# Performance work log

Hardware: AMD Instinct MI355X
Metric: run time of the kernel (lower is better)

## Reference

```python
import jax, jax.numpy as jnp
import numpy as np

D_MODEL = 1024
NUM_HEADS = 16
D_K = D_MODEL // NUM_HEADS


def setup_inputs() -> dict:
    key = jax.random.key(0)
    ks = jax.random.split(key, 7)
    B, S = 4, 2048
    lim = float(np.sqrt(6.0 / (D_MODEL + D_MODEL)))  # xavier uniform
    x = jax.random.normal(ks[0], (B, S, D_MODEL), dtype=jnp.float32)
    w_q = jax.random.uniform(ks[1], (D_MODEL, D_MODEL), jnp.float32, -lim, lim)
    w_k = jax.random.uniform(ks[2], (D_MODEL, D_MODEL), jnp.float32, -lim, lim)
    w_v = jax.random.uniform(ks[3], (D_MODEL, D_MODEL), jnp.float32, -lim, lim)
    w_o = jax.random.uniform(ks[4], (D_MODEL, D_MODEL), jnp.float32, -lim, lim)
    b_o = jnp.zeros((D_MODEL,), jnp.float32)
    ln_g = jnp.ones((D_MODEL,), jnp.float32)
    ln_b = jnp.zeros((D_MODEL,), jnp.float32)
    return {"x": x, "w_q": w_q, "w_k": w_k, "w_v": w_v, "w_o": w_o,
            "b_o": b_o, "ln_g": ln_g, "ln_b": ln_b}


def _layer_norm(y, g, b, eps=1e-5):
    mu = jnp.mean(y, axis=-1, keepdims=True)
    var = jnp.var(y, axis=-1, keepdims=True)
    return (y - mu) * jax.lax.rsqrt(var + eps) * g + b


def reference(x, w_q, w_k, w_v, w_o, b_o, ln_g, ln_b):
    B, S, D = x.shape
    # Linear weights stored torch-style [out, in]: y = x @ W^T
    def proj(w):
        return jnp.einsum('bsd,ed->bse', x, w).reshape(B, S, NUM_HEADS, D_K).transpose(0, 2, 1, 3)
    Q, K, V = proj(w_q), proj(w_k), proj(w_v)  # [B, H, S, d_k]
    scores = jnp.einsum('bhqd,bhkd->bhqk', Q, K) / jnp.sqrt(jnp.float32(D_K))
    attn = jax.nn.softmax(scores, axis=-1)  # dropout identity at eval
    out = jnp.einsum('bhqk,bhkd->bhqd', attn, V)  # [B, H, S, d_k]
    out = out.transpose(0, 2, 1, 3).reshape(B, S, D)
    out = jnp.einsum('bsd,ed->bse', out, w_o) + b_o
    return _layer_norm(x + out, ln_g, ln_b)
```

## Files before the change

kernel.cpp:

```cpp
#include <hip/hip_runtime.h>

typedef __bf16 bf16;
typedef bf16 v8bf __attribute__((ext_vector_type(8)));
typedef bf16 v4bf __attribute__((ext_vector_type(4)));
typedef float v4f __attribute__((ext_vector_type(4)));
typedef float v16f __attribute__((ext_vector_type(16)));
typedef unsigned int u32;
typedef u32 v4u __attribute__((ext_vector_type(4)));

#define GAS __attribute__((address_space(1)))
#define LAS __attribute__((address_space(3)))

constexpr int D    = 1024;
constexpr int ROWS = 8192;
constexpr int TILE = 128;

__global__ __launch_bounds__(256) void cast_all(
    const float* __restrict__ x,
    const float* __restrict__ wq, const float* __restrict__ wk,
    const float* __restrict__ wv, const float* __restrict__ wo,
    bf16* __restrict__ xb, bf16* __restrict__ wqb, bf16* __restrict__ wkb,
    bf16* __restrict__ wvb, bf16* __restrict__ wob)
{
    int i = blockIdx.x * 256 + threadIdx.x;
    const float* src; bf16* dst; int off;
    if (i < 2 * 1024 * 1024) { src = x; dst = xb; off = i; }
    else {
        int j = i - 2 * 1024 * 1024;
        int w = j >> 18;
        off = j & ((1 << 18) - 1);
        src = (w == 0) ? wq : (w == 1) ? wk : (w == 2) ? wv : wo;
        dst = (w == 0) ? wqb : (w == 1) ? wkb : (w == 2) ? wvb : wob;
    }
    float4 v = ((const float4*)src)[off];
    v4bf o;
    o[0] = (bf16)v.x; o[1] = (bf16)v.y; o[2] = (bf16)v.z; o[3] = (bf16)v.w;
    ((v4bf*)dst)[off] = o;
}

template<int MODE>
__global__ __launch_bounds__(256) void gemm_bt(
    const bf16* __restrict__ A,
    const bf16* __restrict__ W0, const bf16* __restrict__ W1, const bf16* __restrict__ W2,
    bf16* __restrict__ O0, bf16* __restrict__ O1, bf16* __restrict__ O2,
    float* __restrict__ Of, const float* __restrict__ bias,
    const float* __restrict__ X)
{
    __shared__ bf16 As[2][TILE * 32];
    __shared__ bf16 Bs[2][TILE * 32];

    const int tid  = threadIdx.x;
    const int lane = tid & 63;
    const int wave = tid >> 6;
    const int quad = lane >> 4;
    const int l16  = lane & 15;
    const int wm   = (wave >> 1) * 64;
    const int wn   = (wave & 1) * 64;

    const int z = blockIdx.z;
    const bf16* Bw = (MODE == 0) ? ((z == 0) ? W0 : ((z == 1) ? W1 : W2)) : W0;
    bf16*       Ob = (MODE == 0) ? ((z == 0) ? O0 : ((z == 1) ? O1 : O2)) : O0;

    const long rowA0 = (long)blockIdx.y * TILE;
    const long rowB0 = (long)blockIdx.x * TILE;

    const int stRow = wave * 16 + (lane >> 2);
    const int stCol = (lane & 3) * 8;
    const bf16* gA = A  + (rowA0 + stRow) * D + stCol;
    const bf16* gB = Bw + (rowB0 + stRow) * D + stCol;
    const int ldsOff = wave * 16 * 32;

    const v4f vzero = {0.f, 0.f, 0.f, 0.f};
    v4f acc[4][4];
    #pragma unroll
    for (int i = 0; i < 4; i++)
        #pragma unroll
        for (int j = 0; j < 4; j++) acc[i][j] = vzero;

    for (int k0 = 0; k0 < D; k0 += 64) {
        __syncthreads();
        #pragma unroll
        for (int p = 0; p < 2; ++p)
            #pragma unroll
            for (int i = 0; i < 2; ++i) {
                __builtin_amdgcn_global_load_lds(
                    (const GAS void*)(gA + (long)i * 64 * D + p * 32),
                    (LAS void*)(&As[p][ldsOff + i * 64 * 32]), 16, 0, 0);
                __builtin_amdgcn_global_load_lds(
                    (const GAS void*)(gB + (long)i * 64 * D + p * 32),
                    (LAS void*)(&Bs[p][ldsOff + i * 64 * 32]), 16, 0, 0);
            }
        gA += 64; gB += 64;
        __syncthreads();

        #pragma unroll
        for (int p = 0; p < 2; ++p) {
            v8bf a[4], b[4];
            #pragma unroll
            for (int mi = 0; mi < 4; mi++)
                a[mi] = *(const v8bf*)(&As[p][(wm + mi * 16 + l16) * 32 + quad * 8]);
            #pragma unroll
            for (int ni = 0; ni < 4; ni++)
                b[ni] = *(const v8bf*)(&Bs[p][(wn + ni * 16 + l16) * 32 + quad * 8]);
            #pragma unroll
            for (int mi = 0; mi < 4; mi++)
                #pragma unroll
                for (int ni = 0; ni < 4; ni++)
                    acc[mi][ni] = __builtin_amdgcn_mfma_f32_16x16x32_bf16(a[mi], b[ni], acc[mi][ni], 0, 0, 0);
        }
    }

    const float qscale = 0.125f * 1.44269504f;

    if (MODE == 0 && z == 2) {
        #pragma unroll
        for (int mi = 0; mi < 4; mi++) {
            #pragma unroll
            for (int ni = 0; ni < 4; ni++) {
                const long col = rowB0 + wn + ni * 16 + l16;
                const long h_ = col >> 6, dd = col & 63;
                const long row0 = rowA0 + wm + mi * 16 + quad * 4;
                const long b_ = row0 >> 11, s0 = row0 & 2047;
                v4bf pk;
                #pragma unroll
                for (int r = 0; r < 4; r++) pk[r] = (bf16)acc[mi][ni][r];
                *(v4bf*)(Ob + ((b_ * 16 + h_) * 64 + dd) * 2048 + s0) = pk;
            }
        }
    } else {
        #pragma unroll
        for (int mi = 0; mi < 4; mi++) {
            #pragma unroll
            for (int ni = 0; ni < 4; ni++) {
                const long col = rowB0 + wn + ni * 16 + l16;
                float bv = (MODE == 1) ? bias[col] : 0.f;
                #pragma unroll
                for (int r = 0; r < 4; r++) {
                    const long row = rowA0 + wm + mi * 16 + quad * 4 + r;
                    float v = acc[mi][ni][r];
                    if (MODE == 1) Of[row * D + col] = v + bv + X[row * D + col];
                    else {
                        if (z == 0) v *= qscale;
                        Ob[row * D + col] = (bf16)v;
                    }
                }
            }
        }
    }
}

__global__ __launch_bounds__(256) void attn_kernel(
    const bf16* __restrict__ Q, const bf16* __restrict__ Kg,
    const bf16* __restrict__ VtG, bf16* __restrict__ O)
{
    const int id  = blockIdx.x;
    const int xcd = id & 7, j = id >> 3;
    const int qt  = j & 15;
    const int g   = xcd + 8 * (j >> 4);
    const int h   = g & 15, b = g >> 4;

    const int tid  = threadIdx.x;
    const int lane = tid & 63;
    const int wave = tid >> 6;
    const int l31  = lane & 31;
    const int hi   = lane >> 5;

    __shared__ bf16 Kt[2][64 * 64];
    __shared__ bf16 Vt[2][64 * 64];

    const long qrow = (long)(b * 2048 + qt * 128 + wave * 32 + l31);
    v8bf qB[4];
    #pragma unroll
    for (int f = 0; f < 4; f++)
        qB[f] = *(const v8bf*)(Q + qrow * D + h * 64 + f * 16 + hi * 8);

    const v16f z16 = {0.f,0.f,0.f,0.f,0.f,0.f,0.f,0.f,
                      0.f,0.f,0.f,0.f,0.f,0.f,0.f,0.f};
    v16f o_acc[2];
    o_acc[0] = z16; o_acc[1] = z16;
    float l0 = 0.f, l1 = 0.f;

    const int iR = tid >> 3;
    const int c8 = tid & 7;
    const int sC = c8 * 8;
    const bf16* kLane = Kg  + (long)b * 2048 * D + h * 64 + sC + (long)iR * D;
    const bf16* vLane = VtG + (long)(b * 16 + h) * 64 * 2048 + sC + (long)iR * 2048;
    const int wOff = iR * 64 + ((c8 ^ (iR & 7)) * 8);

    v8bf kpre[2], vpre[2];
    kpre[0] = *(const v8bf*)(kLane);
    kpre[1] = *(const v8bf*)(kLane + 32 * D);
    vpre[0] = *(const v8bf*)(vLane);
    vpre[1] = *(const v8bf*)(vLane + 32 * 2048);
    kLane += 64 * D; vLane += 64;
    *(v8bf*)(&Kt[0][wOff])           = kpre[0];
    *(v8bf*)(&Kt[0][wOff + 32 * 64]) = kpre[1];
    *(v8bf*)(&Vt[0][wOff])           = vpre[0];
    *(v8bf*)(&Vt[0][wOff + 32 * 64]) = vpre[1];
    kpre[0] = *(const v8bf*)(kLane);
    kpre[1] = *(const v8bf*)(kLane + 32 * D);
    vpre[0] = *(const v8bf*)(vLane);
    vpre[1] = *(const v8bf*)(vLane + 32 * 2048);
    kLane += 64 * D; vLane += 64;

    for (int kt = 0; kt < 32; ++kt) {
        const int cur = kt & 1;
        __syncthreads();

        if (kt + 1 < 32) {
            *(v8bf*)(&Kt[cur ^ 1][wOff])           = kpre[0];
            *(v8bf*)(&Kt[cur ^ 1][wOff + 32 * 64]) = kpre[1];
            *(v8bf*)(&Vt[cur ^ 1][wOff])           = vpre[0];
            *(v8bf*)(&Vt[cur ^ 1][wOff + 32 * 64]) = vpre[1];
        }
        if (kt + 2 < 32) {
            kpre[0] = *(const v8bf*)(kLane);
            kpre[1] = *(const v8bf*)(kLane + 32 * D);
            vpre[0] = *(const v8bf*)(vLane);
            vpre[1] = *(const v8bf*)(vLane + 32 * 2048);
            kLane += 64 * D; vLane += 64;
        }

        #pragma unroll
        for (int ko = 0; ko < 2; ko++) {
            const int krow = ko * 32 + l31;
            const int ksw  = krow & 7;
            v8bf kA0 = *(const v8bf*)(&Kt[cur][krow * 64 + (((0 + hi) ^ ksw) * 8)]);
            v16f st  = __builtin_amdgcn_mfma_f32_32x32x16_bf16(kA0, qB[0], z16, 0, 0, 0);
            #pragma unroll
            for (int f = 1; f < 4; f++) {
                v8bf kA = *(const v8bf*)(&Kt[cur][krow * 64 + (((2 * f + hi) ^ ksw) * 8)]);
                st = __builtin_amdgcn_mfma_f32_32x32x16_bf16(kA, qB[f], st, 0, 0, 0);
            }

            float p[16];
            #pragma unroll
            for (int r = 0; r < 16; r++) {
                p[r] = __builtin_amdgcn_exp2f(st[r]);
                if (r & 1) l1 += p[r]; else l0 += p[r];
            }

            #pragma unroll
            for (int u = 0; u < 2; u++) {
                const int s = ko * 2 + u;
                u32 a0, a1, b0, b1;
                asm("v_cvt_pk_bf16_f32 %0, %1, %2" : "=v"(a0) : "v"(p[u*8+0]), "v"(p[u*8+1]));
                asm("v_cvt_pk_bf16_f32 %0, %1, %2" : "=v"(a1) : "v"(p[u*8+2]), "v"(p[u*8+3]));
                asm("v_cvt_pk_bf16_f32 %0, %1, %2" : "=v"(b0) : "v"(p[u*8+4]), "v"(p[u*8+5]));
                asm("v_cvt_pk_bf16_f32 %0, %1, %2" : "=v"(b1) : "v"(p[u*8+6]), "v"(p[u*8+7]));
                asm("v_permlane32_swap_b32 %0, %1" : "+v"(a0), "+v"(b0));
                asm("v_permlane32_swap_b32 %0, %1" : "+v"(a1), "+v"(b1));
                v4u w; w[0] = a0; w[1] = a1; w[2] = b0; w[3] = b1;
                const v8bf pa = __builtin_bit_cast(v8bf, w);
                #pragma unroll
                for (int d2 = 0; d2 < 2; d2++) {
                    const int vrow = d2 * 32 + l31;
                    v8bf vb = *(const v8bf*)(&Vt[cur][vrow * 64 + (((2 * s + hi) ^ (vrow & 7)) * 8)]);
                    o_acc[d2] = __builtin_amdgcn_mfma_f32_32x32x16_bf16(pa, vb, o_acc[d2], 0, 0, 0);
                }
            }
        }
    }

    float l_acc = l0 + l1;
    l_acc += __shfl_xor(l_acc, 32);

    const long obase = (long)(b * 2048 + qt * 128 + wave * 32);
    #pragma unroll
    for (int r = 0; r < 16; r++) {
        const int qp = (r & 3) + 8 * (r >> 2) + 4 * hi;
        const float inv = 1.f / __shfl(l_acc, qp);
        O[(obase + qp) * D + h * 64 + l31]      = (bf16)(o_acc[0][r] * inv);
        O[(obase + qp) * D + h * 64 + 32 + l31] = (bf16)(o_acc[1][r] * inv);
    }
}

__global__ __launch_bounds__(256) void ln_kernel(
    const float* __restrict__ g, const float* __restrict__ beta,
    float* __restrict__ out)
{
    const int row = blockIdx.x;
    const int t = threadIdx.x;
    const int lane = t & 63, wave = t >> 6;
    const long base = (long)row * D + t * 4;

    float4 yv = *(const float4*)(out + base);
    float y0 = yv.x, y1 = yv.y, y2 = yv.z, y3 = yv.w;
    float s1 = y0 + y1 + y2 + y3;
    float s2 = y0*y0 + y1*y1 + y2*y2 + y3*y3;
    #pragma unroll
    for (int off = 1; off < 64; off <<= 1) {
        s1 += __shfl_xor(s1, off);
        s2 += __shfl_xor(s2, off);
    }
    __shared__ float r1[4], r2[4];
    if (lane == 0) { r1[wave] = s1; r2[wave] = s2; }
    __syncthreads();
    float S1 = r1[0] + r1[1] + r1[2] + r1[3];
    float S2 = r2[0] + r2[1] + r2[2] + r2[3];
    float mu  = S1 * (1.f / 1024.f);
    float var = S2 * (1.f / 1024.f) - mu * mu;
    float rsd = rsqrtf(var + 1e-5f);

    float4 gv = *(const float4*)(g + t * 4);
    float4 bv = *(const float4*)(beta + t * 4);
    float4 o;
    o.x = (y0 - mu) * rsd * gv.x + bv.x;
    o.y = (y1 - mu) * rsd * gv.y + bv.y;
    o.z = (y2 - mu) * rsd * gv.z + bv.z;
    o.w = (y3 - mu) * rsd * gv.w + bv.w;
    *(float4*)(out + base) = o;
}

extern "C" void kernel_launch(void* const* d_in, const int* in_sizes, int n_in,
                              void* d_out, int out_size, void* d_ws, size_t ws_size,
                              hipStream_t stream)
{
    const float* x   = (const float*)d_in[0];
    const float* wq  = (const float*)d_in[1];
    const float* wk  = (const float*)d_in[2];
    const float* wv  = (const float*)d_in[3];
    const float* wo  = (const float*)d_in[4];
    const float* bo  = (const float*)d_in[5];
    const float* lng = (const float*)d_in[6];
    const float* lnb = (const float*)d_in[7];
    float* out = (float*)d_out;

    char* ws = (char*)d_ws;
    bf16* xb  = (bf16*)(ws);
    bf16* wqb = (bf16*)(ws + (size_t)16 * 1024 * 1024);
    bf16* wkb = wqb + 1024 * 1024;
    bf16* wvb = wkb + 1024 * 1024;
    bf16* wob = wvb + 1024 * 1024;
    bf16* Qb  = (bf16*)(ws + (size_t)24 * 1024 * 1024);
    bf16* Kb  = Qb + (size_t)ROWS * D;
    bf16* VtG = Kb + (size_t)ROWS * D;
    bf16* Ab  = VtG + (size_t)ROWS * D;

    cast_all<<<12288, 256, 0, stream>>>(x, wq, wk, wv, wo,
                                        xb, wqb, wkb, wvb, wob);

    dim3 gqkv(D / TILE, ROWS / TILE, 3);
    gemm_bt<0><<<gqkv, 256, 0, stream>>>(xb, wqb, wkb, wvb, Qb, Kb, VtG,
                                         nullptr, nullptr, nullptr);

    attn_kernel<<<dim3(1024, 1, 1), 256, 0, stream>>>(Qb, Kb, VtG, Ab);

    dim3 gout(D / TILE, ROWS / TILE, 1);
    gemm_bt<1><<<gout, 256, 0, stream>>>(Ab, wob, nullptr, nullptr,
                                         nullptr, nullptr, nullptr, out, bo, x);

    ln_kernel<<<8192, 256, 0, stream>>>(lng, lnb, out);
}
```

Measured before the change: 299.9 us.

## Enlarge attention blocks to 512 threads, process two KV tiles per sync

The attention kernel now runs 512-thread blocks covering 256 query rows, so each K/V tile loaded into shared memory is reused by twice as many waves. The grid is halved to match. The loop is restructured so each barrier stages two 64-key tiles into a four-slot buffer, halving synchronisations per KV pass. K fragments are batched before the MFMA chain, and MFMA sections get raised wave priority via s_setprio. The cost is more LDS per block (32 KB) and higher register pressure under launch_bounds(512,4), which may reduce occupancy or cause spills.

```diff
diff --git a/kernel.cpp b/kernel.cpp
--- a/kernel.cpp
+++ b/kernel.cpp
@@ -149,14 +149,14 @@
     }
 }
 
-__global__ __launch_bounds__(256) void attn_kernel(
+__global__ __launch_bounds__(512, 4) void attn_kernel(
     const bf16* __restrict__ Q, const bf16* __restrict__ Kg,
     const bf16* __restrict__ VtG, bf16* __restrict__ O)
 {
     const int id  = blockIdx.x;
     const int xcd = id & 7, j = id >> 3;
-    const int qt  = j & 15;
-    const int g   = xcd + 8 * (j >> 4);
+    const int qt  = j & 7;
+    const int g   = xcd + 8 * (j >> 3);
     const int h   = g & 15, b = g >> 4;
 
     const int tid  = threadIdx.x;
@@ -165,10 +165,10 @@
     const int l31  = lane & 31;
     const int hi   = lane >> 5;
 
-    __shared__ bf16 Kt[2][64 * 64];
-    __shared__ bf16 Vt[2][64 * 64];
-
-    const long qrow = (long)(b * 2048 + qt * 128 + wave * 32 + l31);
+    __shared__ bf16 Kt[4][64 * 64];
+    __shared__ bf16 Vt[4][64 * 64];
+
+    const long qrow = (long)(b * 2048 + qt * 256 + wave * 32 + l31);
     v8bf qB[4];
     #pragma unroll
     for (int f = 0; f < 4; f++)
@@ -182,56 +182,37 @@
 
     const int iR = tid >> 3;
     const int c8 = tid & 7;
-    const int sC = c8 * 8;
-    const bf16* kLane = Kg  + (long)b * 2048 * D + h * 64 + sC + (long)iR * D;
-    const bf16* vLane = VtG + (long)(b * 16 + h) * 64 * 2048 + sC + (long)iR * 2048;
+    const bf16* kLane = Kg  + (long)b * 2048 * D + h * 64 + c8 * 8 + (long)iR * D;
+    const bf16* vLane = VtG + (long)(b * 16 + h) * 64 * 2048 + c8 * 8 + (long)iR * 2048;
     const int wOff = iR * 64 + ((c8 ^ (iR & 7)) * 8);
 
-    v8bf kpre[2], vpre[2];
-    kpre[0] = *(const v8bf*)(kLane);
-    kpre[1] = *(const v8bf*)(kLane + 32 * D);
-    vpre[0] = *(const v8bf*)(vLane);
-    vpre[1] = *(const v8bf*)(vLane + 32 * 2048);
+    v8bf kp[2], vp[2];
+    kp[0] = *(const v8bf*)(kLane); vp[0] = *(const v8bf*)(vLane);
     kLane += 64 * D; vLane += 64;
-    *(v8bf*)(&Kt[0][wOff])           = kpre[0];
-    *(v8bf*)(&Kt[0][wOff + 32 * 64]) = kpre[1];
-    *(v8bf*)(&Vt[0][wOff])           = vpre[0];
-    *(v8bf*)(&Vt[0][wOff + 32 * 64]) = vpre[1];
-    kpre[0] = *(const v8bf*)(kLane);
-    kpre[1] = *(const v8bf*)(kLane + 32 * D);
-    vpre[0] = *(const v8bf*)(vLane);
-    vpre[1] = *(const v8bf*)(vLane + 32 * 2048);
+    kp[1] = *(const v8bf*)(kLane); vp[1] = *(const v8bf*)(vLane);
     kLane += 64 * D; vLane += 64;
-
-    for (int kt = 0; kt < 32; ++kt) {
-        const int cur = kt & 1;
-        __syncthreads();
-
-        if (kt + 1 < 32) {
-            *(v8bf*)(&Kt[cur ^ 1][wOff])           = kpre[0];
-            *(v8bf*)(&Kt[cur ^ 1][wOff + 32 * 64]) = kpre[1];
-            *(v8bf*)(&Vt[cur ^ 1][wOff])           = vpre[0];
-            *(v8bf*)(&Vt[cur ^ 1][wOff + 32 * 64]) = vpre[1];
-        }
-        if (kt + 2 < 32) {
-            kpre[0] = *(const v8bf*)(kLane);
-            kpre[1] = *(const v8bf*)(kLane + 32 * D);
-            vpre[0] = *(const v8bf*)(vLane);
-            vpre[1] = *(const v8bf*)(vLane + 32 * 2048);
-            kLane += 64 * D; vLane += 64;
-        }
-
+    *(v8bf*)(&Kt[0][wOff]) = kp[0]; *(v8bf*)(&Vt[0][wOff]) = vp[0];
+    *(v8bf*)(&Kt[1][wOff]) = kp[1]; *(v8bf*)(&Vt[1][wOff]) = vp[1];
+    kp[0] = *(const v8bf*)(kLane); vp[0] = *(const v8bf*)(vLane);
+    kLane += 64 * D; vLane += 64;
+    kp[1] = *(const v8bf*)(kLane); vp[1] = *(const v8bf*)(vLane);
+    kLane += 64 * D; vLane += 64;
+
+    auto compute = [&](const int bq) {
         #pragma unroll
         for (int ko = 0; ko < 2; ko++) {
             const int krow = ko * 32 + l31;
             const int ksw  = krow & 7;
-            v8bf kA0 = *(const v8bf*)(&Kt[cur][krow * 64 + (((0 + hi) ^ ksw) * 8)]);
-            v16f st  = __builtin_amdgcn_mfma_f32_32x32x16_bf16(kA0, qB[0], z16, 0, 0, 0);
-            #pragma unroll
-            for (int f = 1; f < 4; f++) {
-                v8bf kA = *(const v8bf*)(&Kt[cur][krow * 64 + (((2 * f + hi) ^ ksw) * 8)]);
-                st = __builtin_amdgcn_mfma_f32_32x32x16_bf16(kA, qB[f], st, 0, 0, 0);
-            }
+            v8bf kA[4];
+            #pragma unroll
+            for (int f = 0; f < 4; f++)
+                kA[f] = *(const v8bf*)(&Kt[bq][krow * 64 + (((2 * f + hi) ^ ksw) * 8)]);
+            __builtin_amdgcn_s_setprio(1);
+            v16f st = __builtin_amdgcn_mfma_f32_32x32x16_bf16(kA[0], qB[0], z16, 0, 0, 0);
+            st = __builtin_amdgcn_mfma_f32_32x32x16_bf16(kA[1], qB[1], st, 0, 0, 0);
+            st = __builtin_amdgcn_mfma_f32_32x32x16_bf16(kA[2], qB[2], st, 0, 0, 0);
+            st = __builtin_amdgcn_mfma_f32_32x32x16_bf16(kA[3], qB[3], st, 0, 0, 0);
+            __builtin_amdgcn_s_setprio(0);
 
             float p[16];
             #pragma unroll
@@ -252,20 +233,42 @@
                 asm("v_permlane32_swap_b32 %0, %1" : "+v"(a1), "+v"(b1));
                 v4u w; w[0] = a0; w[1] = a1; w[2] = b0; w[3] = b1;
                 const v8bf pa = __builtin_bit_cast(v8bf, w);
-                #pragma unroll
-                for (int d2 = 0; d2 < 2; d2++) {
-                    const int vrow = d2 * 32 + l31;
-                    v8bf vb = *(const v8bf*)(&Vt[cur][vrow * 64 + (((2 * s + hi) ^ (vrow & 7)) * 8)]);
-                    o_acc[d2] = __builtin_amdgcn_mfma_f32_32x32x16_bf16(pa, vb, o_acc[d2], 0, 0, 0);
-                }
-            }
-        }
+                const int vsw = (l31 & 7);
+                v8bf vb0 = *(const v8bf*)(&Vt[bq][(l31)      * 64 + (((2 * s + hi) ^ vsw) * 8)]);
+                v8bf vb1 = *(const v8bf*)(&Vt[bq][(32 + l31) * 64 + (((2 * s + hi) ^ vsw) * 8)]);
+                __builtin_amdgcn_s_setprio(1);
+                o_acc[0] = __builtin_amdgcn_mfma_f32_32x32x16_bf16(pa, vb0, o_acc[0], 0, 0, 0);
+                o_acc[1] = __builtin_amdgcn_mfma_f32_32x32x16_bf16(pa, vb1, o_acc[1], 0, 0, 0);
+                __builtin_amdgcn_s_setprio(0);
+            }
+        }
+    };
+
+    for (int gg = 0; gg < 16; ++gg) {
+        const int cb = (gg & 1) * 2;
+        __syncthreads();
+
+        if (gg < 15) {
+            *(v8bf*)(&Kt[cb ^ 2][wOff])       = kp[0];
+            *(v8bf*)(&Vt[cb ^ 2][wOff])       = vp[0];
+            *(v8bf*)(&Kt[(cb ^ 2) + 1][wOff]) = kp[1];
+            *(v8bf*)(&Vt[(cb ^ 2) + 1][wOff]) = vp[1];
+        }
+        if (gg < 14) {
+            kp[0] = *(const v8bf*)(kLane); vp[0] = *(const v8bf*)(vLane);
+            kLane += 64 * D; vLane += 64;
+            kp[1] = *(const v8bf*)(kLane); vp[1] = *(const v8bf*)(vLane);
+            kLane += 64 * D; vLane += 64;
+        }
+
+        compute(cb);
+        compute(cb + 1);
     }
 
     float l_acc = l0 + l1;
     l_acc += __shfl_xor(l_acc, 32);
 
-    const long obase = (long)(b * 2048 + qt * 128 + wave * 32);
+    const long obase = (long)(b * 2048 + qt * 256 + wave * 32);
     #pragma unroll
     for (int r = 0; r < 16; r++) {
         const int qp = (r & 3) + 8 * (r >> 2) + 4 * hi;
@@ -344,7 +347,7 @@
     gemm_bt<0><<<gqkv, 256, 0, stream>>>(xb, wqb, wkb, wvb, Qb, Kb, VtG,
                                          nullptr, nullptr, nullptr);
 
-    attn_kernel<<<dim3(1024, 1, 1), 256, 0, stream>>>(Qb, Kb, VtG, Ab);
+    attn_kernel<<<dim3(512, 1, 1), 512, 0, stream>>>(Qb, Kb, VtG, Ab);
 
     dim3 gout(D / TILE, ROWS / TILE, 1);
     gemm_bt<1><<<gout, 256, 0, stream>>>(Ab, wob, nullptr, nullptr,
```

Result: no change. 298.9 us (-0.3%).
